# Kernel optimization log

Measured on AMD Instinct MI355X. Metric: run time of the kernel, lower is better.

The kernel has to match this reference:

```python
import jax, jax.numpy as jnp
import numpy as np

EPS = 1e-4
RES_BAL = 0.3
ATTN_BAL = 0.3
CLIP = 256.0
HEADS = 4
CPH = 64  # channels per head


def _normalize(x, dims):
    # torch normalize: norm = eps + norm * sqrt(norm.numel()/x.numel())
    n = jnp.sqrt(jnp.sum(jnp.square(x), axis=dims, keepdims=True))
    alpha = 1.0 / np.sqrt(float(np.prod([x.shape[d] for d in dims])))
    return x / (EPS + alpha * n)


def _mp_weight(w, gain):
    dims = tuple(range(1, w.ndim))
    fan_in = float(np.prod(w.shape[1:]))
    return _normalize(w, dims) * (gain / np.sqrt(fan_in))


def _conv2d(x, w):
    pad = w.shape[-1] // 2
    return jax.lax.conv_general_dilated(
        x, w, (1, 1), [(pad, pad), (pad, pad)],
        dimension_numbers=('NCHW', 'OIHW', 'NCHW'))


def _mp_silu(x):
    return jax.nn.silu(x) / 0.596


def _mp_sum(a, b, t):
    return ((1.0 - t) * a + t * b) / np.sqrt((1.0 - t) ** 2 + t ** 2)


def setup_inputs() -> dict:
    key = jax.random.key(0)
    ks = jax.random.split(key, 9)
    N, Cin, Cout, Cemb, H, W = 16, 192, 256, 768, 32, 32
    return {
        'x': jax.random.normal(ks[0], (N, Cin, H, W), jnp.float32),
        'emb': jax.random.normal(ks[1], (N, Cemb), jnp.float32),
        'w_skip': jax.random.normal(ks[2], (Cout, Cin, 1, 1), jnp.float32),
        'w_res0': jax.random.normal(ks[3], (Cout, Cout, 3, 3), jnp.float32),
        'w_res1': jax.random.normal(ks[4], (Cout, Cout, 3, 3), jnp.float32),
        'w_emb': jax.random.normal(ks[5], (Cout, Cemb), jnp.float32),
        'emb_gain': jnp.float32(0.5),
        'w_qkv': jax.random.normal(ks[6], (Cout * 3, Cout, 1, 1), jnp.float32),
        'w_proj': jax.random.normal(ks[7], (Cout, Cout, 1, 1), jnp.float32),
    }


def reference(x, emb, w_skip, w_res0, w_res1, w_emb, emb_gain, w_qkv, w_proj):
    N, _, H, W = x.shape
    S = H * W
    # enc flavor: skip conv then pixel-norm over channels
    x = _conv2d(x, _mp_weight(w_skip, 1.0))
    x = _normalize(x, (1,))
    # residual branch
    y = _conv2d(_mp_silu(x), _mp_weight(w_res0, 1.0))
    c = emb @ _mp_weight(w_emb, emb_gain).T + 1.0  # [N, Cout]
    y = y * c[:, :, None, None]
    y = _conv2d(_mp_silu(y), _mp_weight(w_res1, 1.0))
    x = _mp_sum(x, y, RES_BAL)
    # cosine-normalized attention
    qkv = _conv2d(x, _mp_weight(w_qkv, 1.0))              # [N, 3*Cout, H, W]
    qkv = qkv.reshape(N, HEADS, CPH, 3, S)
    qkv = _normalize(qkv, (2,))
    q, k, v = qkv[..., 0, :], qkv[..., 1, :], qkv[..., 2, :]  # [N,h,c,S]
    att = jax.nn.softmax(
        jnp.einsum('nhcq,nhck->nhqk', q, k) / np.sqrt(CPH), axis=3)
    y = jnp.einsum('nhqk,nhck->nhcq', att, v).reshape(x.shape)
    y = _conv2d(y, _mp_weight(w_proj, 1.0))
    x = _mp_sum(x, y, ATTN_BAL)
    return jnp.clip(x, -CLIP, CLIP)
```

## Files before the change

kernel.cpp:

```cpp
#include <hip/hip_runtime.h>
#include <math.h>

#define SDIM 1024
#define COUT 256

#define EPSV     1e-4f
#define SILU_INV 1.6778523489932886f
#define MPA      0.9191450300180579f
#define MPB      0.3939192985791677f
#define LOG2E    1.4426950408889634f

typedef short s16x8 __attribute__((ext_vector_type(8)));
typedef float f32x4 __attribute__((ext_vector_type(4)));
typedef unsigned short ushort_t;

#if __has_builtin(__builtin_amdgcn_exp2f)
#define EXP2F __builtin_amdgcn_exp2f
#else
#define EXP2F exp2f
#endif

__device__ inline ushort_t f2bs(float f) {
    unsigned u = __float_as_uint(f);
    u += 0x7fffu + ((u >> 16) & 1u);
    return (ushort_t)(u >> 16);
}
__device__ inline float silu_mp(float v) { return v * SILU_INV / (1.f + __expf(-v)); }

union F8 { s16x8 v; uint4 q; };
__device__ inline s16x8 ld16(const ushort_t* p) {
    F8 r; r.q = *(const uint4*)p; return r.v;
}

typedef const __attribute__((address_space(1))) unsigned int* gas_ptr;
typedef __attribute__((address_space(3))) unsigned int* las_ptr;
__device__ inline void gld16(const void* g, void* l) {
    __builtin_amdgcn_global_load_lds((gas_ptr)g, (las_ptr)l, 16, 0, 0);
}

__global__ __launch_bounds__(256) void prep_all(
    const float* __restrict__ w_skip, const float* __restrict__ w_res0,
    const float* __restrict__ w_res1, const float* __restrict__ w_qkv,
    const float* __restrict__ w_proj, const float* __restrict__ x,
    ushort_t* wskip_bf, ushort_t* wres0_bf, ushort_t* wres1_bf,
    ushort_t* wqkv_bf, ushort_t* wproj_bf, ushort_t* xT, uint4* zbuf)
{
    __shared__ float T[64 * 65];
    const int b = blockIdx.x, tid = threadIdx.x;

    if (b >= 2560) {
        if (tid < 64) zbuf[tid] = make_uint4(0u, 0u, 0u, 0u);
        return;
    }
    if (b >= 1792) {
        int b2 = b - 1792;
        int n = b2 / 48, rem = b2 % 48;
        int ci0 = (rem / 16) * 64, s0 = (rem & 15) * 64;
#pragma unroll
        for (int i = 0; i < 16; i++) {
            int ch = tid + i * 256; int row = ch >> 6, cc = ch & 63;
            T[row * 65 + cc] = x[((size_t)n * 192 + ci0 + row) * SDIM + s0 + cc];
        }
        __syncthreads();
#pragma unroll
        for (int i = 0; i < 2; i++) {
            int ch = tid + i * 256; int srow = ch >> 3, c8 = ch & 7;
            ushort_t tmp[8];
#pragma unroll
            for (int j = 0; j < 8; j++) tmp[j] = f2bs(T[(c8 * 8 + j) * 65 + srow]);
            *(uint4*)(xT + ((size_t)n * SDIM + s0 + srow) * 192 + ci0 + c8 * 8) = *(uint4*)tmp;
        }
        return;
    }
    const float* src; ushort_t* dst; int fanin, mode, o;
    if      (b < 256)  { src = w_skip; dst = wskip_bf; fanin = 192;  mode = 0; o = b; }
    else if (b < 512)  { src = w_res0; dst = wres0_bf; fanin = 2304; mode = 1; o = b - 256; }
    else if (b < 768)  { src = w_res1; dst = wres1_bf; fanin = 2304; mode = 1; o = b - 512; }
    else if (b < 1536) { src = w_qkv;  dst = wqkv_bf;  fanin = 256;  mode = 2; o = b - 768; }
    else               { src = w_proj; dst = wproj_bf; fanin = 256;  mode = 0; o = b - 1536; }

    const float* row = src + (size_t)o * fanin;
    float ss = 0.f;
    for (int i = tid; i < fanin; i += 256) { float v = row[i]; ss += v * v; }
    for (int off = 32; off >= 1; off >>= 1) ss += __shfl_down(ss, off);
    int lane = tid & 63, wv = tid >> 6;
    if (lane == 0) T[wv] = ss;
    __syncthreads();
    float tot = T[0] + T[1] + T[2] + T[3];
    float scale = 1.0f / (EPSV * sqrtf((float)fanin) + sqrtf(tot));
    int orow = o;
    if (mode == 2) { int h = o / 192, rem = o % 192; orow = (rem % 3) * 256 + h * 64 + rem / 3; }
    for (int i = tid; i < fanin; i += 256) {
        int kd = i;
        if (mode == 1) { int ci = i / 9; int r9 = i - ci * 9; kd = r9 * 256 + ci; }
        dst[(size_t)orow * fanin + kd] = f2bs(row[i] * scale);
    }
}

__global__ __launch_bounds__(256) void emb_mm(const float* __restrict__ emb,
                                              const float* __restrict__ w_emb,
                                              const float* __restrict__ gain_ptr,
                                              float* __restrict__ cvec)
{
    int n = blockIdx.x;
    int co = threadIdx.x;
    const float* e  = emb   + (size_t)n * 768;
    const float* wr = w_emb + (size_t)co * 768;
    float ss = 0.f, dot = 0.f;
    for (int i = 0; i < 768; i++) {
        float wv = wr[i];
        ss  = fmaf(wv, wv, ss);
        dot = fmaf(e[i], wv, dot);
    }
    float scale = gain_ptr[0] / (EPSV * sqrtf(768.0f) + sqrtf(ss));
    cvec[n * COUT + co] = dot * scale + 1.0f;
}

__global__ __launch_bounds__(256, 2) void skip_fused(const ushort_t* __restrict__ Wp,
                                                     const ushort_t* __restrict__ xT,
                                                     float* __restrict__ xn,
                                                     ushort_t* __restrict__ sxT)
{
    const int n = blockIdx.z, s0 = blockIdx.x * 32;
    const int tid = threadIdx.x, w = tid >> 6, lane = tid & 63;
    const int tx = lane & 15, quad = lane >> 4;

    __shared__ ushort_t As[256 * 72];
    __shared__ ushort_t Bs[32 * 72];
    __shared__ float csum[4][32];

    f32x4 acc[4][2];
#pragma unroll
    for (int a = 0; a < 4; a++)
#pragma unroll
        for (int b = 0; b < 2; b++) acc[a][b] = (f32x4){0.f, 0.f, 0.f, 0.f};

    for (int k0 = 0; k0 < 192; k0 += 64) {
        __syncthreads();
#pragma unroll
        for (int i = 0; i < 8; i++) {
            int ch = tid + i * 256; int row = ch >> 3, c8 = ch & 7;
            *(uint4*)&As[row * 72 + c8 * 8] = *(const uint4*)(Wp + (size_t)row * 192 + k0 + c8 * 8);
        }
        {
            int row = tid >> 3, c8 = tid & 7;
            *(uint4*)&Bs[row * 72 + c8 * 8] =
                *(const uint4*)(xT + ((size_t)n * SDIM + s0 + row) * 192 + k0 + c8 * 8);
        }
        __syncthreads();
#pragma unroll
        for (int kc = 0; kc < 2; kc++) {
            s16x8 af[4], bf_[2];
#pragma unroll
            for (int mt = 0; mt < 4; mt++) af[mt] = ld16(&As[(w * 64 + mt * 16 + tx) * 72 + kc * 32 + quad * 8]);
#pragma unroll
            for (int nt = 0; nt < 2; nt++) bf_[nt] = ld16(&Bs[(nt * 16 + tx) * 72 + kc * 32 + quad * 8]);
#pragma unroll
            for (int mt = 0; mt < 4; mt++)
#pragma unroll
                for (int nt = 0; nt < 2; nt++)
                    acc[mt][nt] = __builtin_amdgcn_mfma_f32_16x16x32_bf16(af[mt], bf_[nt], acc[mt][nt], 0, 0, 0);
        }
    }

#pragma unroll
    for (int nt = 0; nt < 2; nt++) {
        float s2 = 0.f;
#pragma unroll
        for (int mt = 0; mt < 4; mt++)
#pragma unroll
            for (int r = 0; r < 4; r++) s2 = fmaf(acc[mt][nt][r], acc[mt][nt][r], s2);
        s2 += __shfl_xor(s2, 16); s2 += __shfl_xor(s2, 32);
        if (quad == 0) csum[w][nt * 16 + tx] = s2;
    }
    __syncthreads();
    float f[2];
#pragma unroll
    for (int nt = 0; nt < 2; nt++) {
        int col = nt * 16 + tx;
        float tot = csum[0][col] + csum[1][col] + csum[2][col] + csum[3][col];
        f[nt] = 1.f / (EPSV + sqrtf(tot) * 0.0625f);
    }
    ushort_t* Ls = As;
    float* xb = xn + (size_t)n * COUT * SDIM;
#pragma unroll
    for (int mt = 0; mt < 4; mt++)
#pragma unroll
        for (int r = 0; r < 4; r++) {
            int co = w * 64 + mt * 16 + quad * 4 + r;
#pragma unroll
            for (int nt = 0; nt < 2; nt++) {
                int sp = s0 + nt * 16 + tx;
                float v = acc[mt][nt][r] * f[nt];
                xb[(size_t)co * SDIM + sp] = v;
                Ls[(nt * 16 + tx) * 264 + co] = f2bs(silu_mp(v));
            }
        }
    __syncthreads();
#pragma unroll
    for (int i = 0; i < 4; i++) {
        int ch = tid + i * 256; int row = ch >> 5, c32 = ch & 31;
        *(uint4*)(sxT + ((size_t)n * SDIM + s0 + row) * 256 + c32 * 8) = *(uint4*)&Ls[row * 264 + c32 * 8];
    }
}

template<int KDIM, bool GATHER3, int MODE>
__global__ __launch_bounds__(256, 2) void gemm_glds(const ushort_t* __restrict__ Wp,
                                                    const ushort_t* __restrict__ Bsrc,
                                                    const ushort_t* __restrict__ zbuf,
                                                    float* RX, float* Outf,
                                                    ushort_t* OutT, ushort_t* Vout,
                                                    const float* __restrict__ cvec)
{
    const int n = blockIdx.z, co0 = blockIdx.y * 128, s0 = blockIdx.x * 64;
    const int tid = threadIdx.x, w = tid >> 6, lane = tid & 63;
    const int tx = lane & 15, quad = lane >> 4;
    const int wm = w >> 1, ws = w & 1;
    const int l8 = lane & 7, ld = lane >> 3;
    const int swz = (l8 ^ ld) * 8;

    __shared__ ushort_t SH[2 * 12288];

    const ushort_t* bn = Bsrc + (size_t)n * SDIM * 256;

    auto stageA = [&](int p, int k0) {
        ushort_t* Ab = SH + p * 12288;
#pragma unroll
        for (int j = 0; j < 4; j++) {
            int row0 = w * 32 + j * 8;
            gld16(Wp + (size_t)(co0 + row0 + ld) * KDIM + k0 + swz, Ab + row0 * 64);
        }
    };
    auto stageB = [&](int p, int k0) {
        ushort_t* Bb = SH + p * 12288 + 8192;
        int ci0 = k0, dy = 0, dx = 0;
        if (GATHER3) { int seg = k0 >> 8; ci0 = k0 & 255; int s3 = seg / 3; dy = s3 - 1; dx = seg - s3 * 3 - 1; }
#pragma unroll
        for (int j = 0; j < 2; j++) {
            int row0 = w * 16 + j * 8;
            const ushort_t* g;
            if (GATHER3) {
                int pix = s0 + row0 + ld;
                int h = (pix >> 5) + dy, wx = (pix & 31) + dx;
                bool valid = ((unsigned)h < 32u) && ((unsigned)wx < 32u);
                g = valid ? (bn + (size_t)((h << 5) + wx) * 256 + ci0 + swz) : zbuf;
            } else {
                g = bn + (size_t)(s0 + row0 + ld) * 256 + k0 + swz;
            }
            gld16(g, Bb + row0 * 64);
        }
    };

    f32x4 acc[4][2];
#pragma unroll
    for (int a = 0; a < 4; a++)
#pragma unroll
        for (int b = 0; b < 2; b++) acc[a][b] = (f32x4){0.f, 0.f, 0.f, 0.f};

    constexpr int NK = KDIM / 64;
    stageA(0, 0); stageB(0, 0);
    __syncthreads();

    for (int kt = 0; kt < NK; kt++) {
        int p = kt & 1;
        if (kt + 1 < NK) { stageA(p ^ 1, (kt + 1) * 64); stageB(p ^ 1, (kt + 1) * 64); }
        const ushort_t* Ab = SH + p * 12288;
        const ushort_t* Bb = Ab + 8192;
#pragma unroll
        for (int kc = 0; kc < 2; kc++) {
            int koff = ((kc * 4 + quad) ^ (tx & 7)) * 8;
            s16x8 af[4], bfv[2];
#pragma unroll
            for (int mt = 0; mt < 4; mt++) af[mt]  = ld16(&Ab[(wm * 64 + mt * 16 + tx) * 64 + koff]);
#pragma unroll
            for (int nt = 0; nt < 2; nt++) bfv[nt] = ld16(&Bb[(ws * 32 + nt * 16 + tx) * 64 + koff]);
#pragma unroll
            for (int mt = 0; mt < 4; mt++)
#pragma unroll
                for (int nt = 0; nt < 2; nt++)
                    acc[mt][nt] = __builtin_amdgcn_mfma_f32_16x16x32_bf16(af[mt], bfv[nt], acc[mt][nt], 0, 0, 0);
        }
        __syncthreads();
    }

    if (MODE == 4) {
        float scl[2];
#pragma unroll
        for (int nt = 0; nt < 2; nt++) {
            float s2 = 0.f;
#pragma unroll
            for (int mt = 0; mt < 4; mt++)
#pragma unroll
                for (int r = 0; r < 4; r++) s2 = fmaf(acc[mt][nt][r], acc[mt][nt][r], s2);
            s2 += __shfl_xor(s2, 16); s2 += __shfl_xor(s2, 32);
            float fac = (co0 < 256) ? (0.125f * LOG2E) : 1.0f;
            scl[nt] = fac / (EPSV + sqrtf(s2) * 0.125f);
        }
#pragma unroll
        for (int mt = 0; mt < 4; mt++)
#pragma unroll
            for (int nt = 0; nt < 2; nt++)
#pragma unroll
                for (int r = 0; r < 4; r++) acc[mt][nt][r] *= scl[nt];

        if (co0 < 512) {
            ushort_t* Ls = SH;
#pragma unroll
            for (int mt = 0; mt < 4; mt++)
#pragma unroll
                for (int nt = 0; nt < 2; nt++)
#pragma unroll
                    for (int r = 0; r < 4; r++)
                        Ls[(ws * 32 + nt * 16 + tx) * 136 + wm * 64 + mt * 16 + quad * 4 + r] = f2bs(acc[mt][nt][r]);
            __syncthreads();
#pragma unroll
            for (int i = 0; i < 4; i++) {
                int ch = tid + i * 256; int row = ch >> 4, c16 = ch & 15;
                *(uint4*)(OutT + ((size_t)n * SDIM + s0 + row) * 512 + co0 + c16 * 8) = *(uint4*)&Ls[row * 136 + c16 * 8];
            }
        } else {
            ushort_t* Ls = SH;
#pragma unroll
            for (int mt = 0; mt < 4; mt++)
#pragma unroll
                for (int nt = 0; nt < 2; nt++)
#pragma unroll
                    for (int r = 0; r < 4; r++)
                        Ls[(wm * 64 + mt * 16 + quad * 4 + r) * 72 + ws * 32 + nt * 16 + tx] = f2bs(acc[mt][nt][r]);
            __syncthreads();
#pragma unroll
            for (int i = 0; i < 4; i++) {
                int ch = tid + i * 256; int row = ch >> 3, c8 = ch & 7;
                *(uint4*)(Vout + ((size_t)n * 256 + (co0 - 512) + row) * SDIM + s0 + c8 * 8) = *(uint4*)&Ls[row * 72 + c8 * 8];
            }
        }
    }
    if (MODE == 1) {
        float cm[4][4];
#pragma unroll
        for (int mt = 0; mt < 4; mt++)
#pragma unroll
            for (int r = 0; r < 4; r++)
                cm[mt][r] = cvec[n * COUT + co0 + wm * 64 + mt * 16 + quad * 4 + r];
        ushort_t* Ls = SH;
#pragma unroll
        for (int mt = 0; mt < 4; mt++)
#pragma unroll
            for (int nt = 0; nt < 2; nt++)
#pragma unroll
                for (int r = 0; r < 4; r++) {
                    float v = silu_mp(acc[mt][nt][r] * cm[mt][r]);
                    Ls[(ws * 32 + nt * 16 + tx) * 136 + wm * 64 + mt * 16 + quad * 4 + r] = f2bs(v);
                }
        __syncthreads();
#pragma unroll
        for (int i = 0; i < 4; i++) {
            int ch = tid + i * 256; int row = ch >> 4, c16 = ch & 15;
            *(uint4*)(OutT + ((size_t)n * SDIM + s0 + row) * 256 + co0 + c16 * 8) = *(uint4*)&Ls[row * 136 + c16 * 8];
        }
    }
    if (MODE == 2) {
        ushort_t* Ls = SH;
#pragma unroll
        for (int mt = 0; mt < 4; mt++)
#pragma unroll
            for (int r = 0; r < 4; r++) {
                int col = wm * 64 + mt * 16 + quad * 4 + r;
                float* xp = RX + ((size_t)n * COUT + co0 + col) * SDIM + s0 + ws * 32;
#pragma unroll
                for (int nt = 0; nt < 2; nt++) {
                    float v = MPA * xp[nt * 16 + tx] + MPB * acc[mt][nt][r];
                    xp[nt * 16 + tx] = v;
                    Ls[(ws * 32 + nt * 16 + tx) * 136 + col] = f2bs(v);
                }
            }
        __syncthreads();
#pragma unroll
        for (int i = 0; i < 4; i++) {
            int ch = tid + i * 256; int row = ch >> 4, c16 = ch & 15;
            *(uint4*)(OutT + ((size_t)n * SDIM + s0 + row) * 256 + co0 + c16 * 8) = *(uint4*)&Ls[row * 136 + c16 * 8];
        }
    }
    if (MODE == 3) {
#pragma unroll
        for (int mt = 0; mt < 4; mt++)
#pragma unroll
            for (int r = 0; r < 4; r++) {
                int co = co0 + wm * 64 + mt * 16 + quad * 4 + r;
                const float* xp = RX + ((size_t)n * COUT + co) * SDIM + s0 + ws * 32;
                float* op = Outf + ((size_t)n * COUT + co) * SDIM + s0 + ws * 32;
#pragma unroll
                for (int nt = 0; nt < 2; nt++) {
                    float v = MPA * xp[nt * 16 + tx] + MPB * acc[mt][nt][r];
                    op[nt * 16 + tx] = fminf(fmaxf(v, -256.f), 256.f);
                }
            }
    }
}

__global__ __launch_bounds__(256, 2) void attn_mfma(const ushort_t* __restrict__ qkT,
                                                    const ushort_t* __restrict__ vbuf,
                                                    ushort_t* __restrict__ aT)
{
    const int n = blockIdx.z, head = blockIdx.y, q0 = blockIdx.x * 128;
    const int tid = threadIdx.x, w = tid >> 6, lane = tid & 63;
    const int tx = lane & 15, quad = lane >> 4;
    const int l8 = lane & 7, ld = lane >> 3;
    const int swz = (l8 ^ ld) * 8;

    __shared__ ushort_t Kst[2][4096];
    __shared__ ushort_t Vst[2][4096];
    __shared__ ushort_t Pw[8][2048];

    const size_t nb = (size_t)n * SDIM;
    const int qw = q0 + w * 32;
    const ushort_t* kg = qkT + nb * 512 + 256 + head * 64;
    const ushort_t* vg = vbuf + ((size_t)n * 256 + head * 64) * SDIM;

    auto stage = [&](int p, int k0) {
#pragma unroll
        for (int j = 0; j < 2; j++) {
            int row0 = w * 16 + j * 8;
            gld16(kg + (size_t)(k0 + row0 + ld) * 512 + swz, &Kst[p][row0 * 64]);
            gld16(vg + (size_t)(row0 + ld) * SDIM + k0 + swz, &Vst[p][row0 * 64]);
        }
    };
    auto pv_step = [&](int pb, f32x4 (&acco)[2][4]) {
        const ushort_t* Pp = Pw[w * 2 + pb];
#pragma unroll
        for (int kc = 0; kc < 2; kc++) {
            int koff = ((kc * 4 + quad) ^ (tx & 7)) * 8;
            s16x8 pf[2];
#pragma unroll
            for (int mt = 0; mt < 2; mt++)
                pf[mt] = ld16(&Pp[(mt * 16 + tx) * 64 + koff]);
#pragma unroll
            for (int nt = 0; nt < 4; nt++) {
                s16x8 vf = ld16(&Vst[pb][(nt * 16 + tx) * 64 + koff]);
#pragma unroll
                for (int mt = 0; mt < 2; mt++)
                    acco[mt][nt] = __builtin_amdgcn_mfma_f32_16x16x32_bf16(
                        pf[mt], vf, acco[mt][nt], 0, 0, 0);
            }
        }
    };

    s16x8 qf[2][2];
#pragma unroll
    for (int mt = 0; mt < 2; mt++)
#pragma unroll
        for (int kc = 0; kc < 2; kc++)
            qf[mt][kc] = ld16(qkT + (nb + qw + mt * 16 + tx) * 512 + head * 64 + kc * 32 + quad * 8);

    f32x4 acco[2][4];
    float lpart[2][4];
#pragma unroll
    for (int mt = 0; mt < 2; mt++)
#pragma unroll
        for (int nt = 0; nt < 4; nt++) acco[mt][nt] = (f32x4){0.f, 0.f, 0.f, 0.f};
#pragma unroll
    for (int mt = 0; mt < 2; mt++)
#pragma unroll
        for (int r = 0; r < 4; r++) lpart[mt][r] = 0.f;

    stage(0, 0);

    for (int kt = 0; kt < 16; kt++) {
        int p = kt & 1;
        if (kt > 0) pv_step(p ^ 1, acco);
        __syncthreads();
        if (kt < 15) stage(p ^ 1, (kt + 1) * 64);

        f32x4 accs[2][4];
#pragma unroll
        for (int mt = 0; mt < 2; mt++)
#pragma unroll
            for (int nt = 0; nt < 4; nt++) accs[mt][nt] = (f32x4){0.f, 0.f, 0.f, 0.f};
#pragma unroll
        for (int kc = 0; kc < 2; kc++) {
            int koff = ((kc * 4 + quad) ^ (tx & 7)) * 8;
#pragma unroll
            for (int nt = 0; nt < 4; nt++) {
                s16x8 kf = ld16(&Kst[p][(nt * 16 + tx) * 64 + koff]);
#pragma unroll
                for (int mt = 0; mt < 2; mt++)
                    accs[mt][nt] = __builtin_amdgcn_mfma_f32_16x16x32_bf16(
                        qf[mt][kc], kf, accs[mt][nt], 0, 0, 0);
            }
        }
#pragma unroll
        for (int mt = 0; mt < 2; mt++)
#pragma unroll
            for (int r = 0; r < 4; r++) {
                int row = mt * 16 + quad * 4 + r;
                int rx = row & 7;
#pragma unroll
                for (int nt = 0; nt < 4; nt++) {
                    float pv = EXP2F(accs[mt][nt][r]);
                    lpart[mt][r] += pv;
                    int slot = (nt * 2 + (tx >> 3)) ^ rx;
                    Pw[w * 2 + p][row * 64 + slot * 8 + (tx & 7)] = f2bs(pv);
                }
            }
    }
    asm volatile("s_waitcnt lgkmcnt(0)" ::: "memory");
    pv_step(1, acco);

    float inv[2][4];
#pragma unroll
    for (int mt = 0; mt < 2; mt++)
#pragma unroll
        for (int r = 0; r < 4; r++) {
            float l = lpart[mt][r];
            l += __shfl_xor(l, 1); l += __shfl_xor(l, 2);
            l += __shfl_xor(l, 4); l += __shfl_xor(l, 8);
            inv[mt][r] = 1.0f / l;
        }

#pragma unroll
    for (int mt = 0; mt < 2; mt++)
#pragma unroll
        for (int r = 0; r < 4; r++) {
            int row = mt * 16 + quad * 4 + r;
            int rx = row & 7;
#pragma unroll
            for (int nt = 0; nt < 4; nt++) {
                int slot = (nt * 2 + (tx >> 3)) ^ rx;
                Pw[w * 2][row * 64 + slot * 8 + (tx & 7)] = f2bs(acco[mt][nt][r] * inv[mt][r]);
            }
        }
    asm volatile("s_waitcnt lgkmcnt(0)" ::: "memory");
    ushort_t* dst = aT + (nb + qw) * 256 + head * 64;
#pragma unroll
    for (int i = 0; i < 4; i++) {
        int ch = lane + i * 64; int row = ch >> 3, c8 = ch & 7;
        *(uint4*)(dst + (size_t)row * 256 + c8 * 8) = *(uint4*)&Pw[w * 2][row * 64 + (c8 ^ (row & 7)) * 8];
    }
}

extern "C" void kernel_launch(void* const* d_in, const int* in_sizes, int n_in,
                              void* d_out, int out_size, void* d_ws, size_t ws_size,
                              hipStream_t stream)
{
    const float* x      = (const float*)d_in[0];
    const float* emb    = (const float*)d_in[1];
    const float* w_skip = (const float*)d_in[2];
    const float* w_res0 = (const float*)d_in[3];
    const float* w_res1 = (const float*)d_in[4];
    const float* w_emb  = (const float*)d_in[5];
    const float* e_gain = (const float*)d_in[6];
    const float* w_qkv  = (const float*)d_in[7];
    const float* w_proj = (const float*)d_in[8];
    float* out = (float*)d_out;

    char* p = (char*)d_ws;
    auto alloc = [&](size_t bytes) { void* r = (void*)p; p += (bytes + 255) & ~(size_t)255; return r; };
    ushort_t* wskip_bf = (ushort_t*)alloc(256 * 192 * 2);
    ushort_t* wres0_bf = (ushort_t*)alloc(256 * 2304 * 2);
    ushort_t* wres1_bf = (ushort_t*)alloc(256 * 2304 * 2);
    ushort_t* wqkv_bf  = (ushort_t*)alloc(768 * 256 * 2);
    ushort_t* wproj_bf = (ushort_t*)alloc(256 * 256 * 2);
    float*    cvec     = (float*)alloc(16 * 256 * 4);
    ushort_t* zbuf     = (ushort_t*)alloc(1024);
    ushort_t* xT   = (ushort_t*)alloc((size_t)16 * 1024 * 192 * 2);
    ushort_t* sxT  = (ushort_t*)alloc((size_t)16 * 1024 * 256 * 2);
    ushort_t* ysT  = (ushort_t*)alloc((size_t)16 * 1024 * 256 * 2);
    ushort_t* x2T  = (ushort_t*)alloc((size_t)16 * 1024 * 256 * 2);
    ushort_t* aT   = (ushort_t*)alloc((size_t)16 * 1024 * 256 * 2);
    float*    xn   = (float*)alloc((size_t)16 * 256 * 1024 * 4);
    ushort_t* qkT  = (ushort_t*)alloc((size_t)16 * 1024 * 512 * 2);
    ushort_t* vbuf = (ushort_t*)alloc((size_t)16 * 256 * 1024 * 2);

    prep_all<<<2561, 256, 0, stream>>>(w_skip, w_res0, w_res1, w_qkv, w_proj, x,
                                       wskip_bf, wres0_bf, wres1_bf, wqkv_bf, wproj_bf,
                                       xT, (uint4*)zbuf);
    emb_mm<<<16, 256, 0, stream>>>(emb, w_emb, e_gain, cvec);

    skip_fused<<<dim3(32, 1, 16), 256, 0, stream>>>(wskip_bf, xT, xn, sxT);
    gemm_glds<2304, true, 1><<<dim3(16, 2, 16), 256, 0, stream>>>(wres0_bf, sxT, zbuf, nullptr, nullptr, ysT, nullptr, cvec);
    gemm_glds<2304, true, 2><<<dim3(16, 2, 16), 256, 0, stream>>>(wres1_bf, ysT, zbuf, xn, nullptr, x2T, nullptr, nullptr);
    gemm_glds<256, false, 4><<<dim3(16, 6, 16), 256, 0, stream>>>(wqkv_bf, x2T, zbuf, nullptr, nullptr, qkT, vbuf, nullptr);
    attn_mfma<<<dim3(8, 4, 16), 256, 0, stream>>>(qkT, vbuf, aT);
    gemm_glds<256, false, 3><<<dim3(16, 2, 16), 256, 0, stream>>>(wproj_bf, aT, zbuf, xn, out, nullptr, nullptr, nullptr);
}
```

Before: 254.6 us.

## Replace LDS-staged double-buffered GEMM with direct global-to-register MFMA operand loads

The GEMM kernels no longer stage weight and activation tiles through double-buffered shared memory via global-to-LDS loads. Each lane now loads its MFMA operand fragments straight from global memory every k-step, and shared memory is kept only for the epilogue transpose. This removes the per-tile barriers and LDS traffic and shrinks shared memory use. In exchange, data reuse across waves now depends on L1/L2 instead of LDS, so the same weight and activation rows are fetched by several waves and the global loads are less coalesced.

```diff
diff --git a/kernel.cpp b/kernel.cpp
--- a/kernel.cpp
+++ b/kernel.cpp
@@ -205,82 +205,63 @@
 }
 
 template<int KDIM, bool GATHER3, int MODE>
-__global__ __launch_bounds__(256, 2) void gemm_glds(const ushort_t* __restrict__ Wp,
-                                                    const ushort_t* __restrict__ Bsrc,
-                                                    const ushort_t* __restrict__ zbuf,
-                                                    float* RX, float* Outf,
-                                                    ushort_t* OutT, ushort_t* Vout,
-                                                    const float* __restrict__ cvec)
+__global__ __launch_bounds__(256, 2) void gemm_direct(const ushort_t* __restrict__ Wp,
+                                                      const ushort_t* __restrict__ Bsrc,
+                                                      const ushort_t* __restrict__ zbuf,
+                                                      float* RX, float* Outf,
+                                                      ushort_t* OutT, ushort_t* Vout,
+                                                      const float* __restrict__ cvec)
 {
     const int n = blockIdx.z, co0 = blockIdx.y * 128, s0 = blockIdx.x * 64;
     const int tid = threadIdx.x, w = tid >> 6, lane = tid & 63;
     const int tx = lane & 15, quad = lane >> 4;
     const int wm = w >> 1, ws = w & 1;
-    const int l8 = lane & 7, ld = lane >> 3;
-    const int swz = (l8 ^ ld) * 8;
-
-    __shared__ ushort_t SH[2 * 12288];
+
+    __shared__ ushort_t Ls[9216];
 
     const ushort_t* bn = Bsrc + (size_t)n * SDIM * 256;
-
-    auto stageA = [&](int p, int k0) {
-        ushort_t* Ab = SH + p * 12288;
-#pragma unroll
-        for (int j = 0; j < 4; j++) {
-            int row0 = w * 32 + j * 8;
-            gld16(Wp + (size_t)(co0 + row0 + ld) * KDIM + k0 + swz, Ab + row0 * 64);
-        }
-    };
-    auto stageB = [&](int p, int k0) {
-        ushort_t* Bb = SH + p * 12288 + 8192;
-        int ci0 = k0, dy = 0, dx = 0;
-        if (GATHER3) { int seg = k0 >> 8; ci0 = k0 & 255; int s3 = seg / 3; dy = s3 - 1; dx = seg - s3 * 3 - 1; }
-#pragma unroll
-        for (int j = 0; j < 2; j++) {
-            int row0 = w * 16 + j * 8;
-            const ushort_t* g;
-            if (GATHER3) {
-                int pix = s0 + row0 + ld;
+    const ushort_t* arow[4];
+#pragma unroll
+    for (int mt = 0; mt < 4; mt++)
+        arow[mt] = Wp + (size_t)(co0 + wm * 64 + mt * 16 + tx) * KDIM;
+    const int pix0 = s0 + ws * 32 + tx;
+
+    f32x4 acc[4][2];
+#pragma unroll
+    for (int a = 0; a < 4; a++)
+#pragma unroll
+        for (int b = 0; b < 2; b++) acc[a][b] = (f32x4){0.f, 0.f, 0.f, 0.f};
+
+    constexpr int NKC = KDIM / 32;
+#pragma unroll 4
+    for (int kcg = 0; kcg < NKC; kcg++) {
+        const int k = kcg * 32 + quad * 8;
+        s16x8 af[4], bfv[2];
+#pragma unroll
+        for (int mt = 0; mt < 4; mt++) af[mt] = ld16(arow[mt] + k);
+        if (GATHER3) {
+            const int seg = k >> 8;
+            const int ci  = k & 255;
+            const int s3  = seg / 3;
+            const int dy  = s3 - 1, dx = seg - s3 * 3 - 1;
+#pragma unroll
+            for (int nt = 0; nt < 2; nt++) {
+                int pix = pix0 + nt * 16;
                 int h = (pix >> 5) + dy, wx = (pix & 31) + dx;
                 bool valid = ((unsigned)h < 32u) && ((unsigned)wx < 32u);
-                g = valid ? (bn + (size_t)((h << 5) + wx) * 256 + ci0 + swz) : zbuf;
-            } else {
-                g = bn + (size_t)(s0 + row0 + ld) * 256 + k0 + swz;
-            }
-            gld16(g, Bb + row0 * 64);
-        }
-    };
-
-    f32x4 acc[4][2];
-#pragma unroll
-    for (int a = 0; a < 4; a++)
-#pragma unroll
-        for (int b = 0; b < 2; b++) acc[a][b] = (f32x4){0.f, 0.f, 0.f, 0.f};
-
-    constexpr int NK = KDIM / 64;
-    stageA(0, 0); stageB(0, 0);
-    __syncthreads();
-
-    for (int kt = 0; kt < NK; kt++) {
-        int p = kt & 1;
-        if (kt + 1 < NK) { stageA(p ^ 1, (kt + 1) * 64); stageB(p ^ 1, (kt + 1) * 64); }
-        const ushort_t* Ab = SH + p * 12288;
-        const ushort_t* Bb = Ab + 8192;
-#pragma unroll
-        for (int kc = 0; kc < 2; kc++) {
-            int koff = ((kc * 4 + quad) ^ (tx & 7)) * 8;
-            s16x8 af[4], bfv[2];
-#pragma unroll
-            for (int mt = 0; mt < 4; mt++) af[mt]  = ld16(&Ab[(wm * 64 + mt * 16 + tx) * 64 + koff]);
-#pragma unroll
-            for (int nt = 0; nt < 2; nt++) bfv[nt] = ld16(&Bb[(ws * 32 + nt * 16 + tx) * 64 + koff]);
-#pragma unroll
-            for (int mt = 0; mt < 4; mt++)
-#pragma unroll
-                for (int nt = 0; nt < 2; nt++)
-                    acc[mt][nt] = __builtin_amdgcn_mfma_f32_16x16x32_bf16(af[mt], bfv[nt], acc[mt][nt], 0, 0, 0);
-        }
-        __syncthreads();
+                const ushort_t* g = valid ? (bn + (size_t)((h << 5) + wx) * 256 + ci) : zbuf;
+                bfv[nt] = ld16(g);
+            }
+        } else {
+#pragma unroll
+            for (int nt = 0; nt < 2; nt++)
+                bfv[nt] = ld16(bn + (size_t)(pix0 + nt * 16) * 256 + k);
+        }
+#pragma unroll
+        for (int mt = 0; mt < 4; mt++)
+#pragma unroll
+            for (int nt = 0; nt < 2; nt++)
+                acc[mt][nt] = __builtin_amdgcn_mfma_f32_16x16x32_bf16(af[mt], bfv[nt], acc[mt][nt], 0, 0, 0);
     }
 
     if (MODE == 4) {
@@ -304,7 +285,6 @@
                 for (int r = 0; r < 4; r++) acc[mt][nt][r] *= scl[nt];
 
         if (co0 < 512) {
-            ushort_t* Ls = SH;
 #pragma unroll
             for (int mt = 0; mt < 4; mt++)
 #pragma unroll
@@ -319,7 +299,6 @@
                 *(uint4*)(OutT + ((size_t)n * SDIM + s0 + row) * 512 + co0 + c16 * 8) = *(uint4*)&Ls[row * 136 + c16 * 8];
             }
         } else {
-            ushort_t* Ls = SH;
 #pragma unroll
             for (int mt = 0; mt < 4; mt++)
 #pragma unroll
@@ -342,7 +321,6 @@
 #pragma unroll
             for (int r = 0; r < 4; r++)
                 cm[mt][r] = cvec[n * COUT + co0 + wm * 64 + mt * 16 + quad * 4 + r];
-        ushort_t* Ls = SH;
 #pragma unroll
         for (int mt = 0; mt < 4; mt++)
 #pragma unroll
@@ -360,7 +338,6 @@
         }
     }
     if (MODE == 2) {
-        ushort_t* Ls = SH;
 #pragma unroll
         for (int mt = 0; mt < 4; mt++)
 #pragma unroll
@@ -577,9 +554,9 @@
     emb_mm<<<16, 256, 0, stream>>>(emb, w_emb, e_gain, cvec);
 
     skip_fused<<<dim3(32, 1, 16), 256, 0, stream>>>(wskip_bf, xT, xn, sxT);
-    gemm_glds<2304, true, 1><<<dim3(16, 2, 16), 256, 0, stream>>>(wres0_bf, sxT, zbuf, nullptr, nullptr, ysT, nullptr, cvec);
-    gemm_glds<2304, true, 2><<<dim3(16, 2, 16), 256, 0, stream>>>(wres1_bf, ysT, zbuf, xn, nullptr, x2T, nullptr, nullptr);
-    gemm_glds<256, false, 4><<<dim3(16, 6, 16), 256, 0, stream>>>(wqkv_bf, x2T, zbuf, nullptr, nullptr, qkT, vbuf, nullptr);
+    gemm_direct<2304, true, 1><<<dim3(16, 2, 16), 256, 0, stream>>>(wres0_bf, sxT, zbuf, nullptr, nullptr, ysT, nullptr, cvec);
+    gemm_direct<2304, true, 2><<<dim3(16, 2, 16), 256, 0, stream>>>(wres1_bf, ysT, zbuf, xn, nullptr, x2T, nullptr, nullptr);
+    gemm_direct<256, false, 4><<<dim3(16, 6, 16), 256, 0, stream>>>(wqkv_bf, x2T, zbuf, nullptr, nullptr, qkT, vbuf, nullptr);
     attn_mfma<<<dim3(8, 4, 16), 256, 0, stream>>>(qkT, vbuf, aT);
-    gemm_glds<256, false, 3><<<dim3(16, 2, 16), 256, 0, stream>>>(wproj_bf, aT, zbuf, xn, out, nullptr, nullptr, nullptr);
-}
+    gemm_direct<256, false, 3><<<dim3(16, 2, 16), 256, 0, stream>>>(wproj_bf, aT, zbuf, xn, out, nullptr, nullptr, nullptr);
+}
```

New measurement: 415.5 us. 63.2% more time.

## Fold emb matmul into prep kernel and transpose QK MFMA for packed P stores

Applied to the files above, without the earlier changes.

The separate emb_mm launch is removed and its work runs as 16 extra blocks of prep_all, saving one kernel launch. In the attention kernel the QK^T MFMA operands are swapped so each lane holds four consecutive query rows of one key column. This lets the bf16 probabilities go to LDS as one 8-byte store instead of scalar 2-byte stores, and lets the row sum build up in a single register per tile. The final row-sum reduction now uses cross-quad shuffles plus a broadcast shuffle.

```diff
diff --git a/kernel.cpp b/kernel.cpp
--- a/kernel.cpp
+++ b/kernel.cpp
@@ -42,13 +42,29 @@
     const float* __restrict__ w_skip, const float* __restrict__ w_res0,
     const float* __restrict__ w_res1, const float* __restrict__ w_qkv,
     const float* __restrict__ w_proj, const float* __restrict__ x,
+    const float* __restrict__ emb, const float* __restrict__ w_emb,
+    const float* __restrict__ gain_ptr, float* __restrict__ cvec,
     ushort_t* wskip_bf, ushort_t* wres0_bf, ushort_t* wres1_bf,
     ushort_t* wqkv_bf, ushort_t* wproj_bf, ushort_t* xT, uint4* zbuf)
 {
     __shared__ float T[64 * 65];
     const int b = blockIdx.x, tid = threadIdx.x;
 
-    if (b >= 2560) {
+    if (b >= 2561) {
+        int n = b - 2561;
+        const float* e  = emb   + (size_t)n * 768;
+        const float* wr = w_emb + (size_t)tid * 768;
+        float ss = 0.f, dot = 0.f;
+        for (int i = 0; i < 768; i++) {
+            float wv = wr[i];
+            ss  = fmaf(wv, wv, ss);
+            dot = fmaf(e[i], wv, dot);
+        }
+        float scale = gain_ptr[0] / (EPSV * sqrtf(768.0f) + sqrtf(ss));
+        cvec[n * COUT + tid] = dot * scale + 1.0f;
+        return;
+    }
+    if (b == 2560) {
         if (tid < 64) zbuf[tid] = make_uint4(0u, 0u, 0u, 0u);
         return;
     }
@@ -97,25 +113,6 @@
     }
 }
 
-__global__ __launch_bounds__(256) void emb_mm(const float* __restrict__ emb,
-                                              const float* __restrict__ w_emb,
-                                              const float* __restrict__ gain_ptr,
-                                              float* __restrict__ cvec)
-{
-    int n = blockIdx.x;
-    int co = threadIdx.x;
-    const float* e  = emb   + (size_t)n * 768;
-    const float* wr = w_emb + (size_t)co * 768;
-    float ss = 0.f, dot = 0.f;
-    for (int i = 0; i < 768; i++) {
-        float wv = wr[i];
-        ss  = fmaf(wv, wv, ss);
-        dot = fmaf(e[i], wv, dot);
-    }
-    float scale = gain_ptr[0] / (EPSV * sqrtf(768.0f) + sqrtf(ss));
-    cvec[n * COUT + co] = dot * scale + 1.0f;
-}
-
 __global__ __launch_bounds__(256, 2) void skip_fused(const ushort_t* __restrict__ Wp,
                                                      const ushort_t* __restrict__ xT,
                                                      float* __restrict__ xn,
@@ -453,15 +450,11 @@
             qf[mt][kc] = ld16(qkT + (nb + qw + mt * 16 + tx) * 512 + head * 64 + kc * 32 + quad * 8);
 
     f32x4 acco[2][4];
-    float lpart[2][4];
+    float lsum[2] = {0.f, 0.f};
 #pragma unroll
     for (int mt = 0; mt < 2; mt++)
 #pragma unroll
         for (int nt = 0; nt < 4; nt++) acco[mt][nt] = (f32x4){0.f, 0.f, 0.f, 0.f};
-#pragma unroll
-    for (int mt = 0; mt < 2; mt++)
-#pragma unroll
-        for (int r = 0; r < 4; r++) lpart[mt][r] = 0.f;
 
     stage(0, 0);
 
@@ -471,11 +464,11 @@
         __syncthreads();
         if (kt < 15) stage(p ^ 1, (kt + 1) * 64);
 
-        f32x4 accs[2][4];
-#pragma unroll
-        for (int mt = 0; mt < 2; mt++)
-#pragma unroll
-            for (int nt = 0; nt < 4; nt++) accs[mt][nt] = (f32x4){0.f, 0.f, 0.f, 0.f};
+        f32x4 accs[4][2];
+#pragma unroll
+        for (int nt = 0; nt < 4; nt++)
+#pragma unroll
+            for (int mt = 0; mt < 2; mt++) accs[nt][mt] = (f32x4){0.f, 0.f, 0.f, 0.f};
 #pragma unroll
         for (int kc = 0; kc < 2; kc++) {
             int koff = ((kc * 4 + quad) ^ (tx & 7)) * 8;
@@ -484,38 +477,38 @@
                 s16x8 kf = ld16(&Kst[p][(nt * 16 + tx) * 64 + koff]);
 #pragma unroll
                 for (int mt = 0; mt < 2; mt++)
-                    accs[mt][nt] = __builtin_amdgcn_mfma_f32_16x16x32_bf16(
-                        qf[mt][kc], kf, accs[mt][nt], 0, 0, 0);
+                    accs[nt][mt] = __builtin_amdgcn_mfma_f32_16x16x32_bf16(
+                        kf, qf[mt][kc], accs[nt][mt], 0, 0, 0);
             }
         }
 #pragma unroll
         for (int mt = 0; mt < 2; mt++)
 #pragma unroll
-            for (int r = 0; r < 4; r++) {
-                int row = mt * 16 + quad * 4 + r;
-                int rx = row & 7;
-#pragma unroll
-                for (int nt = 0; nt < 4; nt++) {
-                    float pv = EXP2F(accs[mt][nt][r]);
-                    lpart[mt][r] += pv;
-                    int slot = (nt * 2 + (tx >> 3)) ^ rx;
-                    Pw[w * 2 + p][row * 64 + slot * 8 + (tx & 7)] = f2bs(pv);
+            for (int nt = 0; nt < 4; nt++) {
+                ushort_t tmp[4];
+#pragma unroll
+                for (int r = 0; r < 4; r++) {
+                    float pv = EXP2F(accs[nt][mt][r]);
+                    lsum[mt] += pv;
+                    tmp[r] = f2bs(pv);
                 }
+                int slot = (nt * 2 + (quad >> 1)) ^ (tx & 7);
+                int addr = (mt * 16 + tx) * 64 + slot * 8 + (quad & 1) * 4;
+                *(uint2*)&Pw[w * 2 + p][addr] = *(uint2*)tmp;
             }
     }
     asm volatile("s_waitcnt lgkmcnt(0)" ::: "memory");
     pv_step(1, acco);
 
-    float inv[2][4];
-#pragma unroll
-    for (int mt = 0; mt < 2; mt++)
-#pragma unroll
-        for (int r = 0; r < 4; r++) {
-            float l = lpart[mt][r];
-            l += __shfl_xor(l, 1); l += __shfl_xor(l, 2);
-            l += __shfl_xor(l, 4); l += __shfl_xor(l, 8);
-            inv[mt][r] = 1.0f / l;
-        }
+    float linv[2][4];
+#pragma unroll
+    for (int mt = 0; mt < 2; mt++) {
+        float l = lsum[mt];
+        l += __shfl_xor(l, 16); l += __shfl_xor(l, 32);
+#pragma unroll
+        for (int r = 0; r < 4; r++)
+            linv[mt][r] = 1.0f / __shfl(l, quad * 4 + r);
+    }
 
 #pragma unroll
     for (int mt = 0; mt < 2; mt++)
@@ -526,7 +519,7 @@
 #pragma unroll
             for (int nt = 0; nt < 4; nt++) {
                 int slot = (nt * 2 + (tx >> 3)) ^ rx;
-                Pw[w * 2][row * 64 + slot * 8 + (tx & 7)] = f2bs(acco[mt][nt][r] * inv[mt][r]);
+                Pw[w * 2][row * 64 + slot * 8 + (tx & 7)] = f2bs(acco[mt][nt][r] * linv[mt][r]);
             }
         }
     asm volatile("s_waitcnt lgkmcnt(0)" ::: "memory");
@@ -571,10 +564,10 @@
     ushort_t* qkT  = (ushort_t*)alloc((size_t)16 * 1024 * 512 * 2);
     ushort_t* vbuf = (ushort_t*)alloc((size_t)16 * 256 * 1024 * 2);
 
-    prep_all<<<2561, 256, 0, stream>>>(w_skip, w_res0, w_res1, w_qkv, w_proj, x,
+    prep_all<<<2577, 256, 0, stream>>>(w_skip, w_res0, w_res1, w_qkv, w_proj, x,
+                                       emb, w_emb, e_gain, cvec,
                                        wskip_bf, wres0_bf, wres1_bf, wqkv_bf, wproj_bf,
                                        xT, (uint4*)zbuf);
-    emb_mm<<<16, 256, 0, stream>>>(emb, w_emb, e_gain, cvec);
 
     skip_fused<<<dim3(32, 1, 16), 256, 0, stream>>>(wskip_bf, xT, xn, sxT);
     gemm_glds<2304, true, 1><<<dim3(16, 2, 16), 256, 0, stream>>>(wres0_bf, sxT, zbuf, nullptr, nullptr, ysT, nullptr, cvec);
```

New measurement: 243.8 us. 1.04x faster.
